# Kernel optimization log

Measured on AMD Instinct MI355X. Metric: run time of the kernel, lower is better.

The kernel has to match this reference:

```python
import jax, jax.numpy as jnp
import numpy as np

T, B, N_IN, N_RNN = 205, 2048, 33, 256
ALPHA = 0.2        # hp['dt']/hp['tau'] = 20/100
SIGMA_REC = 0.0    # hp['sigma_rec'] = 0 -> noise term vanishes


def setup_inputs() -> dict:
    key = jax.random.key(0)
    k_x, k_w = jax.random.split(key)
    x = jax.random.normal(k_x, (T, B, N_IN), dtype=jnp.float32)
    # kernel = concat([w_in (N_IN,N_RNN), w_rec (N_RNN,N_RNN)]) along axis 0
    kernel = jax.random.normal(k_w, (N_IN + N_RNN, N_RNN), dtype=jnp.float32)
    kernel = kernel / np.float32(np.sqrt(N_IN + N_RNN))  # keep dynamics stable
    bias = jnp.zeros((N_RNN,), dtype=jnp.float32)
    h0 = jnp.zeros((B, N_RNN), dtype=jnp.float32)
    return {"x": x, "kernel": kernel, "bias": bias, "h0": h0}


def reference(x, kernel, bias, h0):
    # Leaky RNN cell (Yang et al. style):
    #   gate = concat([x_t, h]) @ kernel + bias
    #   act  = relu(gate + noise)          (noise = sqrt(2*alpha)*sigma_rec*randn; sigma_rec=0)
    #   h    = (1 - alpha) * h + alpha * act
    def step(h, x_t):
        pre = jnp.concatenate([x_t, h], axis=-1) @ kernel + bias  # [B, N_RNN]
        h_new = (1.0 - ALPHA) * h + ALPHA * jax.nn.relu(pre)
        return h_new, h_new

    _, hs = jax.lax.scan(step, h0, x)  # hs: [T, B, N_RNN]
    return hs
```

## Files before the change

kernel.cpp:

```cpp
#include <hip/hip_runtime.h>
#include <cstddef>

#define T_STEPS 205
#define BATCH   2048
#define NIN     33
#define NRNN    256
#define BB      8
#define NTHREADS 256
#define NTW     4


#define A_STRIDE  264
#define X_BSTRIDE 32
#define X_TSTRIDE (BB * X_BSTRIDE)
#define WS_STRIDE 40

typedef _Float16 half8 __attribute__((ext_vector_type(8)));
typedef float    f32x4 __attribute__((ext_vector_type(4)));
typedef unsigned int uintx2 __attribute__((ext_vector_type(2)));

__device__ __forceinline__ void lds_barrier() {
    asm volatile("s_waitcnt lgkmcnt(0)\n\ts_barrier" ::: "memory");
}

__device__ __forceinline__ float permlane_merge(float a, float b) {
    uintx2 r = __builtin_amdgcn_permlane32_swap(
        __builtin_bit_cast(unsigned int, a),
        __builtin_bit_cast(unsigned int, b), false, false);
    return __builtin_bit_cast(float, r[0]);
}

__device__ __forceinline__ int grow(int kk) {
    return (kk < NRNN) ? (33 + kk) : (kk - NRNN);
}

__global__ __launch_bounds__(NTHREADS, 1)
void leaky_rnn_kernel(const float* __restrict__ x,
                      const float* __restrict__ W,
                      const float* __restrict__ bias,
                      const float* __restrict__ h0,
                      float* __restrict__ out)
{
    __shared__ __align__(16) _Float16 A_lds[2][8 * A_STRIDE];
    __shared__ __align__(16) _Float16 X_lds[T_STEPS * X_TSTRIDE];
    __shared__ __align__(16) float    X32[T_STEPS * BB];

    const int tid  = threadIdx.x;
    const int lane = tid & 63;
    const int wave = tid >> 6;
    const int q    = lane >> 4;
    const int nlo  = lane & 15;
    const int qe   = q & 1;
    const int hi   = lane >> 5;
    const int b0   = blockIdx.x * BB;

    _Float16* Wst = &X_lds[0];
    half8 wfrag[NTW][9];
    {
        const int c = tid;
        #pragma unroll
        for (int kt = 0; kt < 9; ++kt) {
            __syncthreads();
            #pragma unroll
            for (int o = 0; o < 4; ++o) {
                half8 pack;
                #pragma unroll
                for (int i = 0; i < 8; ++i)
                    pack[i] = (_Float16)W[grow(kt * 32 + o * 8 + i) * NRNN + c];
                *(half8*)&Wst[c * WS_STRIDE + o * 8] = pack;
            }
            __syncthreads();
            #pragma unroll
            for (int nt = 0; nt < NTW; ++nt) {
                int n = wave * 64 + nt * 16 + nlo;
                wfrag[nt][kt] = *(const half8*)&Wst[n * WS_STRIDE + q * 8];
            }
        }
        __syncthreads();
    }

    int ecol[2]; float bve[2]; float w32e[2];
    #pragma unroll
    for (int p2 = 0; p2 < 2; ++p2) {
        ecol[p2] = wave * 64 + (2 * p2 + hi) * 16 + nlo;
        bve[p2]  = bias[ecol[p2]];
        w32e[p2] = W[32 * NRNN + ecol[p2]];
    }

    for (int e = tid; e < T_STEPS * 66; e += NTHREADS) {
        int t  = e / 66;
        int r4 = e - t * 66;
        f32x4 v = *(const f32x4*)&x[((size_t)t * BATCH + b0) * NIN + r4 * 4];
        #pragma unroll
        for (int j = 0; j < 4; ++j) {
            int idx = r4 * 4 + j;
            int b   = idx / 33;
            int xi  = idx - b * 33;
            if (xi < 32) X_lds[t * X_TSTRIDE + b * X_BSTRIDE + xi] = (_Float16)v[j];
            else         X32[t * BB + b] = v[j];
        }
    }

    float hreg[2][4];
    #pragma unroll
    for (int p2 = 0; p2 < 2; ++p2)
        #pragma unroll
        for (int r = 0; r < 4; ++r) {
            int b = qe * 4 + r;
            float h = h0[(b0 + b) * NRNN + ecol[p2]];
            hreg[p2][r] = h;
            A_lds[0][b * A_STRIDE + ecol[p2]] = (_Float16)h;
        }
    __syncthreads();

    const int am = nlo & 7;
    int p = 0;
    for (int t = 0; t < T_STEPS; ++t) {
        const _Float16* __restrict__ Ar = A_lds[p];
        _Float16* __restrict__ Aw = A_lds[p ^ 1];
        const _Float16* __restrict__ Xt = &X_lds[t * X_TSTRIDE];

        half8 xf   = *(const half8*)&Xt[am * X_BSTRIDE + q * 8];
        f32x4 x32v = *(const f32x4*)&X32[t * BB + qe * 4];

        f32x4 acc[NTW][2];
        #pragma unroll
        for (int nt = 0; nt < NTW; ++nt)
            #pragma unroll
            for (int s = 0; s < 2; ++s) acc[nt][s] = (f32x4){0.f, 0.f, 0.f, 0.f};

        #pragma unroll
        for (int kt = 0; kt < 8; ++kt) {
            half8 af = *(const half8*)&Ar[am * A_STRIDE + kt * 32 + q * 8];
            #pragma unroll
            for (int nt = 0; nt < NTW; ++nt)
                acc[nt][kt & 1] = __builtin_amdgcn_mfma_f32_16x16x32_f16(af, wfrag[nt][kt], acc[nt][kt & 1], 0, 0, 0);
        }
        #pragma unroll
        for (int nt = 0; nt < NTW; ++nt)
            acc[nt][0] = __builtin_amdgcn_mfma_f32_16x16x32_f16(xf, wfrag[nt][8], acc[nt][0], 0, 0, 0);

        f32x4 s[NTW];
        #pragma unroll
        for (int nt = 0; nt < NTW; ++nt) s[nt] = acc[nt][0] + acc[nt][1];

        float hn_[2][4];
        #pragma unroll
        for (int p2 = 0; p2 < 2; ++p2)
            #pragma unroll
            for (int r = 0; r < 4; ++r) {
                float m   = permlane_merge(s[2 * p2][r], s[2 * p2 + 1][r]);
                float pre = m + bve[p2] + x32v[r] * w32e[p2];
                float hn  = 0.8f * hreg[p2][r] + 0.2f * fmaxf(pre, 0.f);
                hreg[p2][r] = hn;
                hn_[p2][r]  = hn;
                Aw[(qe * 4 + r) * A_STRIDE + ecol[p2]] = (_Float16)hn;
            }

        #pragma unroll
        for (int p2 = 0; p2 < 2; ++p2) {
            float* op = out + ((size_t)t * BATCH + b0 + qe * 4) * NRNN + ecol[p2];
            #pragma unroll
            for (int r = 0; r < 4; ++r)
                __builtin_nontemporal_store(hn_[p2][r], op + (size_t)r * NRNN);
        }

        lds_barrier();
        p ^= 1;
    }
}

extern "C" void kernel_launch(void* const* d_in, const int* in_sizes, int n_in,
                              void* d_out, int out_size, void* d_ws, size_t ws_size,
                              hipStream_t stream) {
    const float* x    = (const float*)d_in[0];
    const float* W    = (const float*)d_in[1];
    const float* bias = (const float*)d_in[2];
    const float* h0   = (const float*)d_in[3];
    float* out = (float*)d_out;

    dim3 grid(BATCH / BB);
    dim3 block(NTHREADS);
    leaky_rnn_kernel<<<grid, block, 0, stream>>>(x, W, bias, h0, out);
}
```

Before: 562.5 us.

## Halve batch per block to four rows and allow two blocks per CU

Each block now handles four batch rows instead of eight, which doubles the grid to 512 blocks. Launch bounds are raised to two blocks per CU. The MFMA A-operand rows are replicated four ways, and the results are merged with two permlane16 swaps plus a permlane32 swap, so each lane owns one output column for four rows. The aim is to fill all CUs (256 blocks underused the 256-CU part) and overlap the serial recurrence of two blocks per CU. The cost is more total MFMA work, since 16-row tiles now carry only four distinct rows, and added register pressure from the two-block bound.

```diff
diff --git a/kernel.cpp b/kernel.cpp
--- a/kernel.cpp
+++ b/kernel.cpp
@@ -5,7 +5,7 @@
 #define BATCH   2048
 #define NIN     33
 #define NRNN    256
-#define BB      8
+#define BB      4
 #define NTHREADS 256
 #define NTW     4
 
@@ -23,10 +23,14 @@
     asm volatile("s_waitcnt lgkmcnt(0)\n\ts_barrier" ::: "memory");
 }
 
-__device__ __forceinline__ float permlane_merge(float a, float b) {
-    uintx2 r = __builtin_amdgcn_permlane32_swap(
-        __builtin_bit_cast(unsigned int, a),
-        __builtin_bit_cast(unsigned int, b), false, false);
+__device__ __forceinline__ float merge4(float a0, float a1, float a2, float a3) {
+    uintx2 t0 = __builtin_amdgcn_permlane16_swap(
+        __builtin_bit_cast(unsigned int, a0),
+        __builtin_bit_cast(unsigned int, a1), false, false);
+    uintx2 t1 = __builtin_amdgcn_permlane16_swap(
+        __builtin_bit_cast(unsigned int, a2),
+        __builtin_bit_cast(unsigned int, a3), false, false);
+    uintx2 r  = __builtin_amdgcn_permlane32_swap(t0[0], t1[0], false, false);
     return __builtin_bit_cast(float, r[0]);
 }
 
@@ -34,14 +38,14 @@
     return (kk < NRNN) ? (33 + kk) : (kk - NRNN);
 }
 
-__global__ __launch_bounds__(NTHREADS, 1)
+__global__ __launch_bounds__(NTHREADS, 2)
 void leaky_rnn_kernel(const float* __restrict__ x,
                       const float* __restrict__ W,
                       const float* __restrict__ bias,
                       const float* __restrict__ h0,
                       float* __restrict__ out)
 {
-    __shared__ __align__(16) _Float16 A_lds[2][8 * A_STRIDE];
+    __shared__ __align__(16) _Float16 A_lds[2][BB * A_STRIDE];
     __shared__ __align__(16) _Float16 X_lds[T_STEPS * X_TSTRIDE];
     __shared__ __align__(16) float    X32[T_STEPS * BB];
 
@@ -50,8 +54,6 @@
     const int wave = tid >> 6;
     const int q    = lane >> 4;
     const int nlo  = lane & 15;
-    const int qe   = q & 1;
-    const int hi   = lane >> 5;
     const int b0   = blockIdx.x * BB;
 
     _Float16* Wst = &X_lds[0];
@@ -79,17 +81,13 @@
         __syncthreads();
     }
 
-    int ecol[2]; float bve[2]; float w32e[2];
-    #pragma unroll
-    for (int p2 = 0; p2 < 2; ++p2) {
-        ecol[p2] = wave * 64 + (2 * p2 + hi) * 16 + nlo;
-        bve[p2]  = bias[ecol[p2]];
-        w32e[p2] = W[32 * NRNN + ecol[p2]];
-    }
+    const int   ecol = wave * 64 + q * 16 + nlo;
+    const float bve  = bias[ecol];
+    const float w32e = W[32 * NRNN + ecol];
 
-    for (int e = tid; e < T_STEPS * 66; e += NTHREADS) {
-        int t  = e / 66;
-        int r4 = e - t * 66;
+    for (int e = tid; e < T_STEPS * 33; e += NTHREADS) {
+        int t  = e / 33;
+        int r4 = e - t * 33;
         f32x4 v = *(const f32x4*)&x[((size_t)t * BATCH + b0) * NIN + r4 * 4];
         #pragma unroll
         for (int j = 0; j < 4; ++j) {
@@ -101,19 +99,16 @@
         }
     }
 
-    float hreg[2][4];
+    float hreg[4];
     #pragma unroll
-    for (int p2 = 0; p2 < 2; ++p2)
-        #pragma unroll
-        for (int r = 0; r < 4; ++r) {
-            int b = qe * 4 + r;
-            float h = h0[(b0 + b) * NRNN + ecol[p2]];
-            hreg[p2][r] = h;
-            A_lds[0][b * A_STRIDE + ecol[p2]] = (_Float16)h;
-        }
+    for (int r = 0; r < 4; ++r) {
+        float h = h0[(b0 + r) * NRNN + ecol];
+        hreg[r] = h;
+        A_lds[0][r * A_STRIDE + ecol] = (_Float16)h;
+    }
     __syncthreads();
 
-    const int am = nlo & 7;
+    const int am = lane & 3;
     int p = 0;
     for (int t = 0; t < T_STEPS; ++t) {
         const _Float16* __restrict__ Ar = A_lds[p];
@@ -121,7 +116,7 @@
         const _Float16* __restrict__ Xt = &X_lds[t * X_TSTRIDE];
 
         half8 xf   = *(const half8*)&Xt[am * X_BSTRIDE + q * 8];
-        f32x4 x32v = *(const f32x4*)&X32[t * BB + qe * 4];
+        f32x4 x32v = *(const f32x4*)&X32[t * BB];
 
         f32x4 acc[NTW][2];
         #pragma unroll
@@ -144,26 +139,21 @@
         #pragma unroll
         for (int nt = 0; nt < NTW; ++nt) s[nt] = acc[nt][0] + acc[nt][1];
 
-        float hn_[2][4];
+        float hn_[4];
         #pragma unroll
-        for (int p2 = 0; p2 < 2; ++p2)
-            #pragma unroll
-            for (int r = 0; r < 4; ++r) {
-                float m   = permlane_merge(s[2 * p2][r], s[2 * p2 + 1][r]);
-                float pre = m + bve[p2] + x32v[r] * w32e[p2];
-                float hn  = 0.8f * hreg[p2][r] + 0.2f * fmaxf(pre, 0.f);
-                hreg[p2][r] = hn;
-                hn_[p2][r]  = hn;
-                Aw[(qe * 4 + r) * A_STRIDE + ecol[p2]] = (_Float16)hn;
-            }
+        for (int r = 0; r < 4; ++r) {
+            float m   = merge4(s[0][r], s[1][r], s[2][r], s[3][r]);
+            float pre = m + bve + x32v[r] * w32e;
+            float hn  = 0.8f * hreg[r] + 0.2f * fmaxf(pre, 0.f);
+            hreg[r] = hn;
+            hn_[r]  = hn;
+            Aw[r * A_STRIDE + ecol] = (_Float16)hn;
+        }
 
+        float* op = out + ((size_t)t * BATCH + b0) * NRNN + ecol;
         #pragma unroll
-        for (int p2 = 0; p2 < 2; ++p2) {
-            float* op = out + ((size_t)t * BATCH + b0 + qe * 4) * NRNN + ecol[p2];
-            #pragma unroll
-            for (int r = 0; r < 4; ++r)
-                __builtin_nontemporal_store(hn_[p2][r], op + (size_t)r * NRNN);
-        }
+        for (int r = 0; r < 4; ++r)
+            __builtin_nontemporal_store(hn_[r], op + (size_t)r * NRNN);
 
         lds_barrier();
         p ^= 1;
```

After: 558.5 us. About the same (-0.7%).
